# Optimization experiments

Measured on AMD Instinct MI355X. Metric: run time of the kernel, lower is better.

## Reference

```python
import jax, jax.numpy as jnp
import numpy as np

B, L, C, H = 2, 4096, 512, 8
DH = C // H


def setup_inputs() -> dict:
    key = jax.random.key(0)
    ks = jax.random.split(key, 6)
    s = 1.0 / np.sqrt(C)
    return {
        "x": jax.random.normal(ks[0], (B, L, C), dtype=jnp.float32),
        "Wq": jax.random.normal(ks[1], (C, C), dtype=jnp.float32) * s,
        "Wk": jax.random.normal(ks[2], (C, C), dtype=jnp.float32) * s,
        "Wv": jax.random.normal(ks[3], (C, C), dtype=jnp.float32) * s,
        "Wo": jax.random.normal(ks[4], (C, C), dtype=jnp.float32) * s,
        "bo": jnp.zeros((C,), dtype=jnp.float32),
    }


def reference(x, Wq, Wk, Wv, Wo, bo):
    # x: [B, L, C]; split heads -> [B, H, L, Dh]
    def heads(t):
        return t.reshape(B, L, H, DH).transpose(0, 2, 1, 3)

    q = heads(x @ Wq)
    k = heads(x @ Wk)
    v = heads(x @ Wv)
    scale = 1.0 / np.sqrt(DH)
    scores = jnp.einsum("bhqd,bhkd->bhqk", q, k) * scale  # [B,H,L,L]
    w = jax.nn.softmax(scores, axis=-1)  # dropout_rate=0.0 -> identity
    att = jnp.einsum("bhqk,bhkd->bhqd", w, v)  # [B,H,L,Dh]
    att = att.transpose(0, 2, 1, 3).reshape(B, L, C)
    return att @ Wo + bo
```

## Files before the change

### kernel.cpp

```cpp
#include <hip/hip_runtime.h>
#include <hip/hip_bf16.h>

typedef __hip_bfloat16 bh;
typedef __attribute__((ext_vector_type(8))) __bf16 bf16x8;
typedef __attribute__((ext_vector_type(4))) float f32x4;
typedef __attribute__((ext_vector_type(4))) int i32x4;
typedef __attribute__((ext_vector_type(4))) short s16x4;

#define NB 2
#define NL 4096
#define NC 512
#define NH 8
#define NDH 64
#define NM (NB * NL)
#define LOG2E 1.4426950408889634f
#define KVBLK 8192

static __device__ __forceinline__ f32x4 mfma_bf16(bf16x8 a, bf16x8 b, f32x4 c) {
    return __builtin_amdgcn_mfma_f32_16x16x32_bf16(a, b, c, 0, 0, 0);
}
static __device__ __forceinline__ f32x4 mfma16(s16x4 a, s16x4 b, f32x4 c) {
    return __builtin_amdgcn_mfma_f32_16x16x16bf16_1k(a, b, c, 0, 0, 0);
}

static __device__ __forceinline__ void st_bf4(bh* dst, float a, float b, float c, float d) {
    bh tmp[4] = {__float2bfloat16(a), __float2bfloat16(b),
                 __float2bfloat16(c), __float2bfloat16(d)};
    *(s16x4*)dst = *(const s16x4*)tmp;
}
static __device__ __forceinline__ s16x4 pk_bf4(float a, float b, float c, float d) {
    bh tmp[4] = {__float2bfloat16(a), __float2bfloat16(b),
                 __float2bfloat16(c), __float2bfloat16(d)};
    return *(const s16x4*)tmp;
}

static __device__ __forceinline__ void gload16(const bh* g, bh* l) {
    __builtin_amdgcn_global_load_lds(
        (const __attribute__((address_space(1))) void*)g,
        (__attribute__((address_space(3))) void*)l,
        16, 0, 0);
}

__global__ __launch_bounds__(64)
void w_prep(const float* __restrict__ Wq, const float* __restrict__ Wk,
            const float* __restrict__ Wv, const float* __restrict__ Wo,
            bh* __restrict__ Wf)
{
    const int lane = threadIdx.x;
    const int quad = lane >> 4, c16 = lane & 15;
    const int k0i = blockIdx.x, nt = blockIdx.y, z = blockIdx.z;
    const float* W = (z == 0) ? Wq : (z == 1) ? Wk : (z == 2) ? Wv : Wo;
    bh* dst = Wf + (((size_t)z * 8 + nt) * 8 + k0i) * 4096;
    #pragma unroll
    for (int kc = 0; kc < 2; kc++)
        #pragma unroll
        for (int fn = 0; fn < 4; fn++) {
            bh tmp[8];
            #pragma unroll
            for (int j = 0; j < 8; j++)
                tmp[j] = __float2bfloat16(
                    W[(size_t)(k0i * 64 + kc * 32 + quad * 8 + j) * 512
                      + nt * 64 + fn * 16 + c16]);
            *(i32x4*)&dst[(kc * 4 + fn) * 512 + lane * 8] = *(const i32x4*)tmp;
        }
}

__global__ __launch_bounds__(256, 2)
void qkv_gemm(const float* __restrict__ x, const bh* __restrict__ Wf,
              bh* __restrict__ Qb, bh* __restrict__ KVf)
{
    __shared__ __align__(16) bh smem[128 * 72 + 3 * 4096];
    bh (*Xs)[72] = (bh(*)[72])smem;
    bh* Wl = smem + 128 * 72;

    const int t = threadIdx.x;
    const int wave = t >> 6, lane = t & 63;
    const int quad = lane >> 4, c16 = lane & 15;
    const int m0 = blockIdx.x * 128;
    const int nt = blockIdx.y;

    f32x4 acc[3][2][4];
    for (int z = 0; z < 3; z++)
        for (int a = 0; a < 2; a++)
            for (int b = 0; b < 4; b++)
                for (int u = 0; u < 4; u++) acc[z][a][b][u] = 0.0f;

    for (int k0i = 0; k0i < 8; k0i++) {
        #pragma unroll
        for (int z = 0; z < 3; z++) {
            const bh* wz = Wf + (((size_t)z * 8 + nt) * 8 + k0i) * 4096;
            #pragma unroll
            for (int r = 0; r < 2; r++) {
                int off = (wave * 2 + r) * 512 + lane * 8;
                gload16(wz + off, &Wl[z * 4096 + off]);
            }
        }
        #pragma unroll
        for (int rep = 0; rep < 8; rep++) {
            int li = t + rep * 256;
            int r = li >> 4, c4 = (li & 15) * 4;
            float4 f = *(const float4*)&x[(size_t)(m0 + r) * 512 + k0i * 64 + c4];
            st_bf4(&Xs[r][c4], f.x, f.y, f.z, f.w);
        }
        __syncthreads();
        #pragma unroll
        for (int kc = 0; kc < 2; kc++) {
            bf16x8 af0 = *(const bf16x8*)&Xs[wave * 32 +      c16][kc * 32 + quad * 8];
            bf16x8 af1 = *(const bf16x8*)&Xs[wave * 32 + 16 + c16][kc * 32 + quad * 8];
            #pragma unroll
            for (int z = 0; z < 3; z++)
                #pragma unroll
                for (int fn = 0; fn < 4; fn++) {
                    bf16x8 bf = *(const bf16x8*)&Wl[z * 4096 + (kc * 4 + fn) * 512 + lane * 8];
                    acc[z][0][fn] = mfma_bf16(af0, bf, acc[z][0][fn]);
                    acc[z][1][fn] = mfma_bf16(af1, bf, acc[z][1][fn]);
                }
        }
        __syncthreads();
    }

    const int h = nt;
    const int b = m0 >> 12;
    const int l0 = m0 & 4095;
    const int bh_i = b * NH + h;
    const int kt0 = l0 >> 6;

    {
        bh* Tq = smem;
        #pragma unroll
        for (int fm = 0; fm < 2; fm++)
            #pragma unroll
            for (int i = 0; i < 4; i++) {
                int ll = wave * 32 + fm * 16 + quad * 4 + i;
                #pragma unroll
                for (int fn = 0; fn < 4; fn++)
                    Tq[ll * 68 + fn * 16 + c16] =
                        __float2bfloat16(acc[0][fm][fn][i] * 0.125f);
            }
        __syncthreads();
        int l = t >> 1, half = t & 1;
        bh* dst = Qb + ((size_t)bh_i * NL + l0 + l) * NDH + half * 32;
        const bh* src = &Tq[l * 68 + half * 32];
        #pragma unroll
        for (int r = 0; r < 4; r++)
            *(i32x4*)(dst + r * 8) = *(const i32x4*)(src + r * 8);
        __syncthreads();
    }

    {
        bh* Tk = smem;
        #pragma unroll
        for (int fm = 0; fm < 2; fm++)
            #pragma unroll
            for (int i = 0; i < 4; i++) {
                int ll = wave * 32 + fm * 16 + quad * 4 + i;
                int ktl = ll >> 6, l64 = ll & 63;
                int fk = l64 >> 4, c16t = l64 & 15;
                #pragma unroll
                for (int fn = 0; fn < 4; fn++) {
                    int d = fn * 16 + c16;
                    int kc = d >> 5, qt = (d >> 3) & 3, j = d & 7;
                    Tk[ktl * 4096 + (fk * 2 + kc) * 512 + (qt * 16 + c16t) * 8 + j] =
                        __float2bfloat16(acc[1][fm][fn][i] * LOG2E);
                }
            }
        __syncthreads();
        int idx = t * 32;
        int ktl = idx >> 12, wi = idx & 4095;
        bh* dst = KVf + (size_t)(bh_i * 64 + kt0 + ktl) * KVBLK + wi;
        #pragma unroll
        for (int r = 0; r < 4; r++)
            *(i32x4*)(dst + r * 8) = *(const i32x4*)&Tk[idx + r * 8];
    }

    #pragma unroll
    for (int fm = 0; fm < 2; fm++) {
        int fkv = (wave * 2 + fm) & 3;
        int ktv = kt0 + (wave >> 1);
        #pragma unroll
        for (int fn = 0; fn < 4; fn++) {
            size_t addr = (size_t)(bh_i * 64 + ktv) * KVBLK + 4096
                        + (size_t)(fn * 4 + fkv) * 256 + (quad * 16 + c16) * 4;
            st_bf4(&KVf[addr], acc[2][fm][fn][0], acc[2][fm][fn][1],
                               acc[2][fm][fn][2], acc[2][fm][fn][3]);
        }
    }
}

__global__ __launch_bounds__(512, 4)
void flash_attn(const bh* __restrict__ Qb, const bh* __restrict__ KVf,
                bh* __restrict__ attb)
{
    __shared__ __align__(16) bh SF[2][2][KVBLK];

    const int t = threadIdx.x;
    const int wave = t >> 6, lane = t & 63;
    const int group = wave >> 2, w4 = wave & 3;
    const int quad = lane >> 4, c16 = lane & 15;
    const int bh_idx = blockIdx.y;
    const int q0 = blockIdx.x * 128;

    const bh* Qp  = Qb + (size_t)bh_idx * NL * NDH;
    const bh* KVp = KVf + (size_t)bh_idx * 64 * KVBLK;

    bf16x8 qf[2][2];
    #pragma unroll
    for (int fq = 0; fq < 2; fq++)
        #pragma unroll
        for (int kc = 0; kc < 2; kc++)
            qf[fq][kc] = *(const bf16x8*)
                &Qp[(size_t)(q0 + w4 * 32 + fq * 16 + c16) * NDH + kc * 32 + quad * 8];

    f32x4 ot[4][2];
    float lsum[2] = {0.0f, 0.0f};
    for (int a = 0; a < 4; a++)
        for (int fq = 0; fq < 2; fq++)
            for (int u = 0; u < 4; u++) ot[a][fq][u] = 0.0f;

    auto stage = [&](int i, int buf) {
        int kt = 2 * i + group;
        #pragma unroll
        for (int r = 0; r < 4; r++) {
            int off = (w4 * 4 + r) * 512 + lane * 8;
            gload16(KVp + (size_t)kt * KVBLK + off, &SF[group][buf][off]);
        }
    };

    stage(0, 0);
    for (int i = 0; i < 32; i++) {
        const int buf = i & 1;
        __syncthreads();
        if (i < 31) stage(i + 1, buf ^ 1);
        const bh* sf = &SF[group][buf][0];

        f32x4 s[4][2];
        for (int a = 0; a < 4; a++)
            for (int fq = 0; fq < 2; fq++)
                for (int u = 0; u < 4; u++) s[a][fq][u] = 0.0f;
        #pragma unroll
        for (int kc = 0; kc < 2; kc++)
            #pragma unroll
            for (int fk = 0; fk < 4; fk++) {
                bf16x8 kf = *(const bf16x8*)&sf[(fk * 2 + kc) * 512 + lane * 8];
                s[fk][0] = mfma_bf16(kf, qf[0][kc], s[fk][0]);
                s[fk][1] = mfma_bf16(kf, qf[1][kc], s[fk][1]);
            }

        s16x4 vt[4][4];
        #pragma unroll
        for (int fn = 0; fn < 4; fn++)
            #pragma unroll
            for (int fk = 0; fk < 4; fk++)
                vt[fn][fk] = *(const s16x4*)&sf[4096 + (fn * 4 + fk) * 256 + lane * 4];

        s16x4 pf[4][2];
        float rs0 = 0.0f, rs1 = 0.0f;
        #pragma unroll
        for (int fk = 0; fk < 4; fk++) {
            float a0 = __builtin_amdgcn_exp2f(s[fk][0][0]);
            float a1 = __builtin_amdgcn_exp2f(s[fk][0][1]);
            float a2 = __builtin_amdgcn_exp2f(s[fk][0][2]);
            float a3 = __builtin_amdgcn_exp2f(s[fk][0][3]);
            rs0 += (a0 + a1) + (a2 + a3);
            pf[fk][0] = pk_bf4(a0, a1, a2, a3);
            float b0 = __builtin_amdgcn_exp2f(s[fk][1][0]);
            float b1 = __builtin_amdgcn_exp2f(s[fk][1][1]);
            float b2 = __builtin_amdgcn_exp2f(s[fk][1][2]);
            float b3 = __builtin_amdgcn_exp2f(s[fk][1][3]);
            rs1 += (b0 + b1) + (b2 + b3);
            pf[fk][1] = pk_bf4(b0, b1, b2, b3);
        }
        lsum[0] += rs0;
        lsum[1] += rs1;

        #pragma unroll
        for (int fk = 0; fk < 4; fk++)
            #pragma unroll
            for (int fn = 0; fn < 4; fn++) {
                ot[fn][0] = mfma16(vt[fn][fk], pf[fk][0], ot[fn][0]);
                ot[fn][1] = mfma16(vt[fn][fk], pf[fk][1], ot[fn][1]);
            }
    }

    #pragma unroll
    for (int fq = 0; fq < 2; fq++) {
        lsum[fq] += __shfl_xor(lsum[fq], 16);
        lsum[fq] += __shfl_xor(lsum[fq], 32);
    }

    float* Ocmb = (float*)&SF[0][0][0];
    float* Lcmb = Ocmb + 128 * 64;
    __syncthreads();
    if (group == 1) {
        #pragma unroll
        for (int fq = 0; fq < 2; fq++) {
            int q = w4 * 32 + fq * 16 + c16;
            #pragma unroll
            for (int fn = 0; fn < 4; fn++)
                *(f32x4*)&Ocmb[q * 64 + fn * 16 + quad * 4] = ot[fn][fq];
            if (quad == 0) Lcmb[q] = lsum[fq];
        }
    }
    __syncthreads();
    if (group == 0) {
        const int b = bh_idx >> 3, h = bh_idx & 7;
        #pragma unroll
        for (int fq = 0; fq < 2; fq++) {
            int q = w4 * 32 + fq * 16 + c16;
            float inv = 1.0f / (lsum[fq] + Lcmb[q]);
            size_t rowbase = ((size_t)b * NL + (q0 + q)) * NC + h * NDH;
            #pragma unroll
            for (int fn = 0; fn < 4; fn++) {
                f32x4 o2 = *(const f32x4*)&Ocmb[q * 64 + fn * 16 + quad * 4];
                st_bf4(&attb[rowbase + fn * 16 + quad * 4],
                       (ot[fn][fq][0] + o2[0]) * inv, (ot[fn][fq][1] + o2[1]) * inv,
                       (ot[fn][fq][2] + o2[2]) * inv, (ot[fn][fq][3] + o2[3]) * inv);
            }
        }
    }
}

__global__ __launch_bounds__(256, 2)
void out_gemm(const bh* __restrict__ A, const bh* __restrict__ Wf,
              const float* __restrict__ bo, float* __restrict__ out)
{
    __shared__ __align__(16) bh Xs[128][72];
    __shared__ __align__(16) bh Wl[4096];

    const int t = threadIdx.x;
    const int wave = t >> 6, lane = t & 63;
    const int quad = lane >> 4, c16 = lane & 15;
    const int m0 = blockIdx.x * 128;
    const int nt = blockIdx.y;
    const int n0 = nt * 64;

    f32x4 acc[2][4];
    for (int a = 0; a < 2; a++)
        for (int b = 0; b < 4; b++)
            for (int u = 0; u < 4; u++) acc[a][b][u] = 0.0f;

    for (int k0i = 0; k0i < 8; k0i++) {
        const bh* wz = Wf + (((size_t)3 * 8 + nt) * 8 + k0i) * 4096;
        #pragma unroll
        for (int r = 0; r < 2; r++) {
            int off = (wave * 2 + r) * 512 + lane * 8;
            gload16(wz + off, &Wl[off]);
        }
        #pragma unroll
        for (int rep = 0; rep < 4; rep++) {
            int li = t + rep * 256;
            int r = li >> 3, d0 = (li & 7) * 8;
            *(i32x4*)&Xs[r][d0] = *(const i32x4*)&A[(size_t)(m0 + r) * 512 + k0i * 64 + d0];
        }
        __syncthreads();
        #pragma unroll
        for (int kc = 0; kc < 2; kc++) {
            bf16x8 af0 = *(const bf16x8*)&Xs[wave * 32 +      c16][kc * 32 + quad * 8];
            bf16x8 af1 = *(const bf16x8*)&Xs[wave * 32 + 16 + c16][kc * 32 + quad * 8];
            #pragma unroll
            for (int fn = 0; fn < 4; fn++) {
                bf16x8 bf = *(const bf16x8*)&Wl[(kc * 4 + fn) * 512 + lane * 8];
                acc[0][fn] = mfma_bf16(af0, bf, acc[0][fn]);
                acc[1][fn] = mfma_bf16(af1, bf, acc[1][fn]);
            }
        }
        __syncthreads();
    }

    #pragma unroll
    for (int fm = 0; fm < 2; fm++)
        #pragma unroll
        for (int i = 0; i < 4; i++) {
            int mr = m0 + wave * 32 + fm * 16 + quad * 4 + i;
            #pragma unroll
            for (int fn = 0; fn < 4; fn++) {
                int cn = n0 + fn * 16 + c16;
                out[(size_t)mr * 512 + cn] = acc[fm][fn][i] + bo[cn];
            }
        }
}

extern "C" void kernel_launch(void* const* d_in, const int* in_sizes, int n_in,
                              void* d_out, int out_size, void* d_ws, size_t ws_size,
                              hipStream_t stream)
{
    const float* x  = (const float*)d_in[0];
    const float* Wq = (const float*)d_in[1];
    const float* Wk = (const float*)d_in[2];
    const float* Wv = (const float*)d_in[3];
    const float* Wo = (const float*)d_in[4];
    const float* bo = (const float*)d_in[5];
    float* out = (float*)d_out;

    const size_t mat = (size_t)NM * NC;
    bh* Qb   = (bh*)d_ws;
    bh* KVf  = Qb + mat;
    bh* attb = KVf + 2 * mat;
    bh* Wf   = attb + mat;

    w_prep    <<<dim3(8, 8, 4),           64, 0, stream>>>(Wq, Wk, Wv, Wo, Wf);
    qkv_gemm  <<<dim3(NM / 128, NC / 64), 256, 0, stream>>>(x, Wf, Qb, KVf);
    flash_attn<<<dim3(NL / 128, NB * NH), 512, 0, stream>>>(Qb, KVf, attb);
    out_gemm  <<<dim3(NM / 128, NC / 64), 256, 0, stream>>>(attb, Wf, bo, out);
}
```

Baseline: 205.1 us.

## Pre-convert x to bf16 MFMA fragment layout in merged prep kernel

Merges the weight prep kernel with a new pass that converts x to bf16 once and stores it in MFMA fragment order. qkv_gemm then loads X tiles with direct global-to-LDS async loads instead of re-reading fp32 x and converting it in each of the 8 column-tile blocks. The occupancy hints for qkv_gemm and out_gemm are also raised. This trades an extra bf16 write and read of x, plus extra workspace, for removing the redundant fp32 reads and conversions, at some risk of register pressure from the higher occupancy targets.

```diff
diff --git a/kernel.cpp b/kernel.cpp
--- a/kernel.cpp
+++ b/kernel.cpp
@@ -41,43 +41,68 @@
         16, 0, 0);
 }
 
-__global__ __launch_bounds__(64)
-void w_prep(const float* __restrict__ Wq, const float* __restrict__ Wk,
-            const float* __restrict__ Wv, const float* __restrict__ Wo,
-            bh* __restrict__ Wf)
+__global__ __launch_bounds__(256, 2)
+void prep(const float* __restrict__ x,
+          const float* __restrict__ Wq, const float* __restrict__ Wk,
+          const float* __restrict__ Wv, const float* __restrict__ Wo,
+          bh* __restrict__ xf, bh* __restrict__ Wf)
 {
-    const int lane = threadIdx.x;
+    const int t = threadIdx.x;
+    const int wave = t >> 6, lane = t & 63;
     const int quad = lane >> 4, c16 = lane & 15;
-    const int k0i = blockIdx.x, nt = blockIdx.y, z = blockIdx.z;
-    const float* W = (z == 0) ? Wq : (z == 1) ? Wk : (z == 2) ? Wv : Wo;
-    bh* dst = Wf + (((size_t)z * 8 + nt) * 8 + k0i) * 4096;
-    #pragma unroll
-    for (int kc = 0; kc < 2; kc++)
-        #pragma unroll
-        for (int fn = 0; fn < 4; fn++) {
-            bh tmp[8];
-            #pragma unroll
-            for (int j = 0; j < 8; j++)
-                tmp[j] = __float2bfloat16(
-                    W[(size_t)(k0i * 64 + kc * 32 + quad * 8 + j) * 512
-                      + nt * 64 + fn * 16 + c16]);
-            *(i32x4*)&dst[(kc * 4 + fn) * 512 + lane * 8] = *(const i32x4*)tmp;
-        }
-}
-
-__global__ __launch_bounds__(256, 2)
-void qkv_gemm(const float* __restrict__ x, const bh* __restrict__ Wf,
+
+    if (blockIdx.z < 8) {
+        __shared__ __align__(16) bh T[64][72];
+        const int m64 = blockIdx.x, k64 = blockIdx.z;
+        #pragma unroll
+        for (int rep = 0; rep < 4; rep++) {
+            int li = t + rep * 256;
+            int r = li >> 4, c4 = (li & 15) * 4;
+            float4 f = *(const float4*)&x[(size_t)(m64 * 64 + r) * 512 + k64 * 64 + c4];
+            st_bf4(&T[r][c4], f.x, f.y, f.z, f.w);
+        }
+        __syncthreads();
+        #pragma unroll
+        for (int kcl = 0; kcl < 2; kcl++) {
+            i32x4 v = *(const i32x4*)&T[wave * 16 + c16][kcl * 32 + quad * 8];
+            size_t addr = ((size_t)(m64 * 4 + wave) * 16 + (k64 * 2 + kcl)) * 512 + lane * 8;
+            *(i32x4*)&xf[addr] = v;
+        }
+    } else {
+        if (blockIdx.x >= 64) return;
+        int task = blockIdx.x * 4 + wave;
+        int z = task >> 6, nt = (task >> 3) & 7, k0i = task & 7;
+        const float* W = (z == 0) ? Wq : (z == 1) ? Wk : (z == 2) ? Wv : Wo;
+        bh* dst = Wf + (((size_t)z * 8 + nt) * 8 + k0i) * 4096;
+        #pragma unroll
+        for (int kc = 0; kc < 2; kc++)
+            #pragma unroll
+            for (int fn = 0; fn < 4; fn++) {
+                bh tmp[8];
+                #pragma unroll
+                for (int j = 0; j < 8; j++)
+                    tmp[j] = __float2bfloat16(
+                        W[(size_t)(k0i * 64 + kc * 32 + quad * 8 + j) * 512
+                          + nt * 64 + fn * 16 + c16]);
+                *(i32x4*)&dst[(kc * 4 + fn) * 512 + lane * 8] = *(const i32x4*)tmp;
+            }
+    }
+}
+
+__global__ __launch_bounds__(256, 3)
+void qkv_gemm(const bh* __restrict__ xf, const bh* __restrict__ Wf,
               bh* __restrict__ Qb, bh* __restrict__ KVf)
 {
-    __shared__ __align__(16) bh smem[128 * 72 + 3 * 4096];
-    bh (*Xs)[72] = (bh(*)[72])smem;
-    bh* Wl = smem + 128 * 72;
+    __shared__ __align__(16) bh smem[8192 + 3 * 4096];
+    bh* Xl = smem;
+    bh* Wl = smem + 8192;
 
     const int t = threadIdx.x;
     const int wave = t >> 6, lane = t & 63;
     const int quad = lane >> 4, c16 = lane & 15;
     const int m0 = blockIdx.x * 128;
     const int nt = blockIdx.y;
+    const int m16b = m0 >> 4;
 
     f32x4 acc[3][2][4];
     for (int z = 0; z < 3; z++)
@@ -87,6 +112,13 @@
 
     for (int k0i = 0; k0i < 8; k0i++) {
         #pragma unroll
+        for (int r = 0; r < 4; r++) {
+            int f = wave * 4 + r;
+            const bh* src = xf + ((size_t)(m16b + (f >> 1)) * 16 + k0i * 2 + (f & 1)) * 512
+                          + lane * 8;
+            gload16(src, &Xl[f * 512 + lane * 8]);
+        }
+        #pragma unroll
         for (int z = 0; z < 3; z++) {
             const bh* wz = Wf + (((size_t)z * 8 + nt) * 8 + k0i) * 4096;
             #pragma unroll
@@ -95,18 +127,11 @@
                 gload16(wz + off, &Wl[z * 4096 + off]);
             }
         }
-        #pragma unroll
-        for (int rep = 0; rep < 8; rep++) {
-            int li = t + rep * 256;
-            int r = li >> 4, c4 = (li & 15) * 4;
-            float4 f = *(const float4*)&x[(size_t)(m0 + r) * 512 + k0i * 64 + c4];
-            st_bf4(&Xs[r][c4], f.x, f.y, f.z, f.w);
-        }
         __syncthreads();
         #pragma unroll
         for (int kc = 0; kc < 2; kc++) {
-            bf16x8 af0 = *(const bf16x8*)&Xs[wave * 32 +      c16][kc * 32 + quad * 8];
-            bf16x8 af1 = *(const bf16x8*)&Xs[wave * 32 + 16 + c16][kc * 32 + quad * 8];
+            bf16x8 af0 = *(const bf16x8*)&Xl[((wave * 2 + 0) * 2 + kc) * 512 + lane * 8];
+            bf16x8 af1 = *(const bf16x8*)&Xl[((wave * 2 + 1) * 2 + kc) * 512 + lane * 8];
             #pragma unroll
             for (int z = 0; z < 3; z++)
                 #pragma unroll
@@ -320,7 +345,7 @@
     }
 }
 
-__global__ __launch_bounds__(256, 2)
+__global__ __launch_bounds__(256, 4)
 void out_gemm(const bh* __restrict__ A, const bh* __restrict__ Wf,
               const float* __restrict__ bo, float* __restrict__ out)
 {
@@ -397,9 +422,10 @@
     bh* KVf  = Qb + mat;
     bh* attb = KVf + 2 * mat;
     bh* Wf   = attb + mat;
-
-    w_prep    <<<dim3(8, 8, 4),           64, 0, stream>>>(Wq, Wk, Wv, Wo, Wf);
-    qkv_gemm  <<<dim3(NM / 128, NC / 64), 256, 0, stream>>>(x, Wf, Qb, KVf);
+    bh* xf   = Wf + 4 * 8 * 8 * 4096;
+
+    prep      <<<dim3(128, 1, 9),         256, 0, stream>>>(x, Wq, Wk, Wv, Wo, xf, Wf);
+    qkv_gemm  <<<dim3(NM / 128, NC / 64), 256, 0, stream>>>(xf, Wf, Qb, KVf);
     flash_attn<<<dim3(NL / 128, NB * NH), 512, 0, stream>>>(Qb, KVf, attb);
     out_gemm  <<<dim3(NM / 128, NC / 64), 256, 0, stream>>>(attb, Wf, bo, out);
 }
```

Measured after the change: 190.5 us. 7.1% less time.
